# Performance work log

Measured on AMD Instinct MI355X. Metric: run time of the kernel, lower is better.

## Reference

```python
import jax, jax.numpy as jnp
import numpy as np

DIM = 2048
N_HEADS = 16
N_KV_HEADS = 4
HEAD_DIM = DIM // N_HEADS


def setup_inputs() -> dict:
    key = jax.random.key(0)
    k1, k2, k3, k4, k5 = jax.random.split(key, 5)
    B, T = 2, 2048
    scale = 1.0 / np.sqrt(DIM)
    x = jax.random.normal(k1, (B, T, DIM), dtype=jnp.float32)
    # weights stored as [in, out] so forward is x @ W (same math as nn.Linear)
    Wq = jax.random.normal(k2, (DIM, DIM), dtype=jnp.float32) * scale
    Wk = jax.random.normal(k3, (DIM, N_KV_HEADS * HEAD_DIM), dtype=jnp.float32) * scale
    Wv = jax.random.normal(k4, (DIM, N_KV_HEADS * HEAD_DIM), dtype=jnp.float32) * scale
    Wo = jax.random.normal(k5, (DIM, DIM), dtype=jnp.float32) * scale
    return {"x": x, "Wq": Wq, "Wk": Wk, "Wv": Wv, "Wo": Wo}


def reference(x, Wq, Wk, Wv, Wo):
    B, T, C = x.shape
    G = N_HEADS // N_KV_HEADS  # query heads per kv head
    # projections
    q = (x @ Wq).reshape(B, T, N_KV_HEADS, G, HEAD_DIM)   # [B,T,K,G,d]
    k = (x @ Wk).reshape(B, T, N_KV_HEADS, HEAD_DIM)      # [B,T,K,d]
    v = (x @ Wv).reshape(B, T, N_KV_HEADS, HEAD_DIM)      # [B,T,K,d]
    # attention scores: grouped heads share kv head (no repeat_interleave copy)
    att = jnp.einsum('btkgd,bskd->bkgts', q, k) / np.sqrt(HEAD_DIM)  # [B,K,G,T,T]
    att = jax.nn.softmax(att, axis=-1)
    out = jnp.einsum('bkgts,bskd->btkgd', att, v).reshape(B, T, C)
    return out @ Wo
```

## Files before the change

### kernel.cpp

```cpp
#include <hip/hip_runtime.h>
#include <hip/hip_bf16.h>

typedef __hip_bfloat16 bf16;
typedef __attribute__((ext_vector_type(8))) short short8;
typedef __attribute__((ext_vector_type(4))) short short4v;
typedef __attribute__((ext_vector_type(4))) float f32x4;

#define DIMC 2048
#define TSEQ 2048
#define NB 2
#define KVH 4
#define NH 16
#define HD 128
#define KVD 512
#define QSCALE 0.12751744f

#if __has_builtin(__builtin_amdgcn_exp2f)
#define EXP2(x) __builtin_amdgcn_exp2f(x)
#else
#define EXP2(x) exp2f(x)
#endif

__device__ __forceinline__ float fmax3(float a, float b, float c) {
  return fmaxf(fmaxf(a, b), c);
}

__device__ __forceinline__ void mfma16(f32x4& acc, short8 a, short8 b) {
  acc = __builtin_amdgcn_mfma_f32_16x16x32_bf16(a, b, acc, 0, 0, 0);
}

__device__ __forceinline__ void gload_lds16(const bf16* g, bf16* l) {
  __builtin_amdgcn_global_load_lds(
      (const __attribute__((address_space(1))) void*)g,
      (__attribute__((address_space(3))) void*)l, 16, 0, 0);
}

__device__ __forceinline__ int swz(int row, int col) {
  return col ^ ((row & 7) << 3);
}

__global__ __launch_bounds__(256) void f2b(const float* __restrict__ in,
                                           bf16* __restrict__ out, long n4) {
  long i = (long)blockIdx.x * 256 + threadIdx.x;
  if (i >= n4) return;
  const f32x4 v = *(const f32x4*)(in + i * 4);
  union { short4v s; bf16 h[4]; } u;
#pragma unroll
  for (int j = 0; j < 4; ++j) u.h[j] = __float2bfloat16(v[j]);
  *(short4v*)(out + i * 4) = u.s;
}

__global__ __launch_bounds__(256) void transpose_all(const float* __restrict__ Wq,
                                                     const float* __restrict__ Wk,
                                                     const float* __restrict__ Wv,
                                                     const float* __restrict__ Wo,
                                                     bf16* __restrict__ WT3,
                                                     bf16* __restrict__ WoT) {
  __shared__ bf16 tile[64][72];
  const int y = blockIdx.y;
  const float* in;
  bf16* out;
  int C, rb, cb;
  float scale = 1.0f;
  if (y < 32) {
    in = Wq; out = WT3; C = 2048;
    rb = y * 64; cb = blockIdx.x * 64; scale = QSCALE;
  } else if (y < 40) {
    in = Wk; out = WT3 + (long)2048 * DIMC; C = 512;
    rb = blockIdx.x * 64; cb = (y - 32) * 64;
  } else if (y < 48) {
    in = Wv; out = WT3 + (long)2560 * DIMC; C = 512;
    rb = blockIdx.x * 64; cb = (y - 40) * 64;
  } else {
    in = Wo; out = WoT; C = 2048;
    rb = (y - 48) * 64; cb = blockIdx.x * 64;
  }
  int tx = threadIdx.x & 63, ty = threadIdx.x >> 6;
  for (int i = ty; i < 64; i += 4)
    tile[i][tx] = __float2bfloat16(in[(long)(rb + i) * C + cb + tx] * scale);
  __syncthreads();
  for (int i = ty; i < 64; i += 4)
    out[(long)(cb + i) * DIMC + rb + tx] = tile[tx][i];
}

#define XCD_REMAP(NX)                                                          \
  const int flat_ = blockIdx.y * (NX) + blockIdx.x;                            \
  const int tot_ = (NX) * gridDim.y;                                           \
  const int log_ = (flat_ & 7) * (tot_ >> 3) + (flat_ >> 3);                   \
  const long m0 = (long)(log_ / (NX)) * 128, n0 = (long)(log_ % (NX)) * 128;

#define GEMM_BODY(A_, Bt_, K_)                                                  \
  const int tid = threadIdx.x;                                                  \
  const int lane = tid & 63, wid = tid >> 6;                                    \
  const int wm = (wid >> 1) * 64, wn = (wid & 1) * 64;                          \
  f32x4 acc[4][4] = {};                                                         \
  const int srow = lane >> 2, scol = (lane & 3) * 8;                            \
  const bf16* Ag = A_ + (m0 + srow) * (long)K_ + scol;                          \
  const bf16* Bg = Bt_ + (n0 + srow) * (long)K_ + scol;                         \
  for (int k0 = 0; k0 < K_; k0 += 32) {                                         \
    for (int p = 0; p < 2; ++p) {                                               \
      int rr = p * 64 + wid * 16;                                               \
      gload_lds16(Ag + (long)rr * K_ + k0, As + rr * 32);                       \
      gload_lds16(Bg + (long)rr * K_ + k0, Bs + rr * 32);                       \
    }                                                                           \
    __syncthreads();                                                            \
    const int ko = (lane >> 4) * 8;                                             \
    short8 af[4], bq[4];                                                        \
    _Pragma("unroll") for (int i = 0; i < 4; ++i) {                             \
      af[i] = *(const short8*)(As + (wm + i * 16 + (lane & 15)) * 32 + ko);     \
      bq[i] = *(const short8*)(Bs + (wn + i * 16 + (lane & 15)) * 32 + ko);     \
    }                                                                           \
    _Pragma("unroll") for (int i = 0; i < 4; ++i)                               \
      _Pragma("unroll") for (int j = 0; j < 4; ++j)                             \
        mfma16(acc[i][j], af[i], bq[j]);                                        \
    __syncthreads();                                                            \
  }                                                                             \
  const int cr = (lane >> 4) * 4, cc = lane & 15;

__global__ __launch_bounds__(256) void gemm_qkv(const bf16* __restrict__ A,
                                                const bf16* __restrict__ Bt,
                                                bf16* __restrict__ qp,
                                                bf16* __restrict__ kp,
                                                bf16* __restrict__ vT) {
  __shared__ bf16 As[128 * 32];
  __shared__ bf16 Bs[128 * 32];
  XCD_REMAP(24)
  GEMM_BODY(A, Bt, 2048)
#pragma unroll
  for (int i = 0; i < 4; ++i)
#pragma unroll
    for (int j = 0; j < 4; ++j)
#pragma unroll
      for (int r = 0; r < 4; ++r) {
        long m = m0 + wm + i * 16 + cr + r;
        long n = n0 + wn + j * 16 + cc;
        float val = acc[i][j][r];
        if (n0 < 2048) {
          qp[m * DIMC + n] = __float2bfloat16(val);
        } else if (n0 < 2560) {
          kp[m * KVD + (n - 2048)] = __float2bfloat16(val);
        } else {
          long nn = n - 2560;
          long z = (m >> 11) * 4 + (nn >> 7);
          vT[z * (HD * (long)TSEQ) + (nn & 127) * (long)TSEQ + (m & 2047)] =
              __float2bfloat16(val);
        }
      }
}

__global__ __launch_bounds__(256) void gemm_out(const bf16* __restrict__ A,
                                                const bf16* __restrict__ Bt,
                                                float* __restrict__ C) {
  __shared__ bf16 As[128 * 32];
  __shared__ bf16 Bs[128 * 32];
  XCD_REMAP(16)
  GEMM_BODY(A, Bt, 2048)
#pragma unroll
  for (int i = 0; i < 4; ++i)
#pragma unroll
    for (int j = 0; j < 4; ++j)
#pragma unroll
      for (int r = 0; r < 4; ++r) {
        long m = m0 + wm + i * 16 + cr + r;
        long n = n0 + wn + j * 16 + cc;
        C[m * DIMC + n] = acc[i][j][r];
      }
}

__global__ __launch_bounds__(256, 2) void attn_fwd(const bf16* __restrict__ Qp,
                                                   const bf16* __restrict__ Kp,
                                                   const bf16* __restrict__ Vt,
                                                   bf16* __restrict__ AO) {
  __shared__ bf16 Ks[2][64 * 128];
  __shared__ bf16 Vts[2][128 * 64];
  const int tid = threadIdx.x;
  const int lane = tid & 63, wid = tid >> 6;
  const int h = blockIdx.y, b = blockIdx.z;
  const int kv = h >> 2;
  const int t0 = blockIdx.x * 128;
  const int lr = lane & 15, lg = lane >> 4;

  short8 aq[2][4];
#pragma unroll
  for (int f = 0; f < 2; ++f) {
    const bf16* qrow =
        Qp + ((long)(b * TSEQ + t0 + wid * 32 + f * 16 + lr)) * DIMC + h * HD + lg * 8;
#pragma unroll
    for (int c = 0; c < 4; ++c) aq[f][c] = *(const short8*)(qrow + c * 32);
  }
  f32x4 o[2][8] = {};
  float mrun[2] = {-1e30f, -1e30f}, lrun[2] = {0.f, 0.f};

  const bf16* Kg = Kp + (long)b * TSEQ * KVD + kv * HD;
  const bf16* Vg = Vt + ((long)(b * KVH + kv)) * HD * TSEQ;

  const int krow = tid >> 2;
  const int vrow = tid >> 1;
  short8 kreg[2][2], vreg[2][2];
#pragma unroll
  for (int s = 0; s < 2; ++s)
#pragma unroll
    for (int p = 0; p < 2; ++p) {
      kreg[s][p] = *(const short8*)(Kg + (long)krow * KVD + (2 * (tid & 3) + s) * 16 + p * 8);
      vreg[s][p] = *(const short8*)(Vg + (long)vrow * TSEQ + (2 * (tid & 1) + s) * 16 + 8 * p);
    }

  for (int s0 = 0; s0 < TSEQ; s0 += 64) {
    const int buf = (s0 >> 6) & 1;
    bf16* Kb = Ks[buf];
    bf16* Vb = Vts[buf];
#pragma unroll
    for (int s = 0; s < 2; ++s)
#pragma unroll
      for (int p = 0; p < 2; ++p) {
        int kc0 = (2 * (tid & 3) + s) * 16;
        *(short8*)(Kb + krow * 128 + swz(krow, kc0 + p * 8)) = kreg[s][p];
        int va = 2 * (tid & 1) + s;
        union { short8 v8; short4v q[2]; } u;
        u.v8 = vreg[s][p];
        int sl1 = (4 * (va >> 1) + 2 * p + vrow) & 7;
        int sl2 = (4 * (va >> 1) + 2 * p + 1 + vrow) & 7;
        int hf = (va & 1) * 4;
        *(short4v*)(Vb + vrow * 64 + sl1 * 8 + hf) = u.q[0];
        *(short4v*)(Vb + vrow * 64 + sl2 * 8 + hf) = u.q[1];
      }
    __syncthreads();
    if (s0 + 64 < TSEQ) {
#pragma unroll
      for (int s = 0; s < 2; ++s)
#pragma unroll
        for (int p = 0; p < 2; ++p) {
          kreg[s][p] = *(const short8*)(Kg + (long)(s0 + 64 + krow) * KVD +
                                        (2 * (tid & 3) + s) * 16 + p * 8);
          vreg[s][p] = *(const short8*)(Vg + (long)vrow * TSEQ + s0 + 64 +
                                        (2 * (tid & 1) + s) * 16 + 8 * p);
        }
    }

    f32x4 sacc[2][4] = {};
    __builtin_amdgcn_s_setprio(1);
#pragma unroll
    for (int sf = 0; sf < 4; ++sf)
#pragma unroll
      for (int c = 0; c < 4; ++c) {
        int row = sf * 16 + lr;
        short8 kf = *(const short8*)(Kb + row * 128 + swz(row, c * 32 + lg * 8));
        mfma16(sacc[0][sf], kf, aq[0][c]);
        mfma16(sacc[1][sf], kf, aq[1][c]);
      }
    __builtin_amdgcn_s_setprio(0);

    union { short8 s; bf16 h[8]; } pb[2][2];
#pragma unroll
    for (int f = 0; f < 2; ++f) {
      float tmax = fmaxf(sacc[f][0][0], sacc[f][0][1]);
      tmax = fmax3(tmax, sacc[f][0][2], sacc[f][0][3]);
      tmax = fmax3(tmax, sacc[f][1][0], sacc[f][1][1]);
      tmax = fmax3(tmax, sacc[f][1][2], sacc[f][1][3]);
      tmax = fmax3(tmax, sacc[f][2][0], sacc[f][2][1]);
      tmax = fmax3(tmax, sacc[f][2][2], sacc[f][2][3]);
      tmax = fmax3(tmax, sacc[f][3][0], sacc[f][3][1]);
      tmax = fmax3(tmax, sacc[f][3][2], sacc[f][3][3]);
      tmax = fmaxf(tmax, __shfl_xor(tmax, 16));
      tmax = fmaxf(tmax, __shfl_xor(tmax, 32));
      if (__any(tmax > mrun[f] + 8.0f)) {
        float mnew = fmaxf(mrun[f], tmax);
        float fac = EXP2(mrun[f] - mnew);
        mrun[f] = mnew;
        lrun[f] *= fac;
#pragma unroll
        for (int df = 0; df < 8; ++df) o[f][df] *= fac;
      }
      float p4[4][4];
      float ps = 0.f;
#pragma unroll
      for (int sf = 0; sf < 4; ++sf)
#pragma unroll
        for (int r = 0; r < 4; ++r) {
          float pv = EXP2(sacc[f][sf][r] - mrun[f]);
          p4[sf][r] = pv;
          ps += pv;
        }
      lrun[f] += ps;
#pragma unroll
      for (int c2 = 0; c2 < 2; ++c2)
#pragma unroll
        for (int r = 0; r < 4; ++r) {
          pb[f][c2].h[r] = __float2bfloat16(p4[2 * c2][r]);
          pb[f][c2].h[4 + r] = __float2bfloat16(p4[2 * c2 + 1][r]);
        }
    }

    __builtin_amdgcn_s_setprio(1);
#pragma unroll
    for (int c2 = 0; c2 < 2; ++c2) {
#pragma unroll
      for (int df = 0; df < 8; ++df) {
        int row = df * 16 + lr;
        short8 vf = *(const short8*)(Vb + row * 64 + ((4 * c2 + lg + row) & 7) * 8);
        mfma16(o[0][df], vf, pb[0][c2].s);
        mfma16(o[1][df], vf, pb[1][c2].s);
      }
    }
    __builtin_amdgcn_s_setprio(0);
  }

#pragma unroll
  for (int f = 0; f < 2; ++f) {
    lrun[f] += __shfl_xor(lrun[f], 16);
    lrun[f] += __shfl_xor(lrun[f], 32);
  }

#pragma unroll
  for (int f = 0; f < 2; ++f) {
    float inv = 1.0f / lrun[f];
    bf16* obase =
        AO + ((long)(b * TSEQ + t0 + wid * 32 + f * 16 + lr)) * DIMC + h * HD + lg * 4;
#pragma unroll
    for (int df = 0; df < 8; ++df) {
      union { short4v s; bf16 h[4]; } ov;
#pragma unroll
      for (int r = 0; r < 4; ++r) ov.h[r] = __float2bfloat16(o[f][df][r] * inv);
      *(short4v*)(obase + df * 16) = ov.s;
    }
  }
}

extern "C" void kernel_launch(void* const* d_in, const int* in_sizes, int n_in,
                              void* d_out, int out_size, void* d_ws, size_t ws_size,
                              hipStream_t stream) {
  const float* x  = (const float*)d_in[0];
  const float* Wq = (const float*)d_in[1];
  const float* Wk = (const float*)d_in[2];
  const float* Wv = (const float*)d_in[3];
  const float* Wo = (const float*)d_in[4];
  float* out = (float*)d_out;
  bf16* ws = (bf16*)d_ws;

  bf16* xb  = ws;
  bf16* WT3 = xb + 8388608;
  bf16* WoT = WT3 + 6291456;
  bf16* qp  = WoT + 4194304;
  bf16* kp  = qp + 8388608;
  bf16* vT  = kp + 2097152;

  f2b<<<8192, 256, 0, stream>>>(x, xb, 2097152);
  transpose_all<<<dim3(32, 80), 256, 0, stream>>>(Wq, Wk, Wv, Wo, WT3, WoT);

  gemm_qkv<<<dim3(24, 32), 256, 0, stream>>>(xb, WT3, qp, kp, vT);

  bf16* ao = xb;
  attn_fwd<<<dim3(16, 16, 2), 256, 0, stream>>>(qp, kp, vT, ao);

  gemm_out<<<dim3(16, 32), 256, 0, stream>>>(ao, WoT, out);
}
```

Before: 221.0 us.

## Deepen GEMM K-tile to 64 with XOR-swizzled LDS and fuse x conversion into transpose

The shared GEMM body now stages a 64-wide K slice per iteration instead of 32. It uses an XOR swizzle on the LDS columns, applied both when loading and when reading, which halves the number of barriers per K and aims to avoid LDS bank conflicts on fragment reads. Separately, the x fp32-to-bf16 conversion is merged into the weight-transpose kernel as extra grid rows, which removes one kernel launch. LDS use per GEMM block doubles, which may reduce occupancy.

```diff
diff --git a/kernel.cpp b/kernel.cpp
--- a/kernel.cpp
+++ b/kernel.cpp
@@ -39,25 +39,29 @@
   return col ^ ((row & 7) << 3);
 }
 
-__global__ __launch_bounds__(256) void f2b(const float* __restrict__ in,
-                                           bf16* __restrict__ out, long n4) {
-  long i = (long)blockIdx.x * 256 + threadIdx.x;
-  if (i >= n4) return;
-  const f32x4 v = *(const f32x4*)(in + i * 4);
-  union { short4v s; bf16 h[4]; } u;
-#pragma unroll
-  for (int j = 0; j < 4; ++j) u.h[j] = __float2bfloat16(v[j]);
-  *(short4v*)(out + i * 4) = u.s;
-}
-
 __global__ __launch_bounds__(256) void transpose_all(const float* __restrict__ Wq,
                                                      const float* __restrict__ Wk,
                                                      const float* __restrict__ Wv,
                                                      const float* __restrict__ Wo,
+                                                     const float* __restrict__ x,
                                                      bf16* __restrict__ WT3,
-                                                     bf16* __restrict__ WoT) {
+                                                     bf16* __restrict__ WoT,
+                                                     bf16* __restrict__ xb) {
+  const int y = blockIdx.y;
+  if (y >= 80) {
+    long base = (((long)(y - 80) * 32 + blockIdx.x) * 2048) + threadIdx.x;
+#pragma unroll
+    for (int j = 0; j < 8; ++j) {
+      long i = base + j * 256;
+      const f32x4 v = *(const f32x4*)(x + i * 4);
+      union { short4v s; bf16 h[4]; } u;
+#pragma unroll
+      for (int k = 0; k < 4; ++k) u.h[k] = __float2bfloat16(v[k]);
+      *(short4v*)(xb + i * 4) = u.s;
+    }
+    return;
+  }
   __shared__ bf16 tile[64][72];
-  const int y = blockIdx.y;
   const float* in;
   bf16* out;
   int C, rb, cb;
@@ -94,25 +98,30 @@
   const int lane = tid & 63, wid = tid >> 6;                                    \
   const int wm = (wid >> 1) * 64, wn = (wid & 1) * 64;                          \
   f32x4 acc[4][4] = {};                                                         \
-  const int srow = lane >> 2, scol = (lane & 3) * 8;                            \
-  const bf16* Ag = A_ + (m0 + srow) * (long)K_ + scol;                          \
-  const bf16* Bg = Bt_ + (n0 + srow) * (long)K_ + scol;                         \
-  for (int k0 = 0; k0 < K_; k0 += 32) {                                         \
-    for (int p = 0; p < 2; ++p) {                                               \
-      int rr = p * 64 + wid * 16;                                               \
-      gload_lds16(Ag + (long)rr * K_ + k0, As + rr * 32);                       \
-      gload_lds16(Bg + (long)rr * K_ + k0, Bs + rr * 32);                       \
+  const int srow = lane >> 3;                  \
+  const int sslot = lane & 7;                           \
+  for (int k0 = 0; k0 < K_; k0 += 64) {                                         \
+    _Pragma("unroll") for (int p = 0; p < 4; ++p) {                             \
+      int rr = p * 32 + wid * 8;                                                \
+      int row = rr + srow;                                                      \
+      int scol = (sslot ^ (row & 7)) * 8;    \
+      gload_lds16(A_ + (m0 + row) * (long)K_ + k0 + scol, As + rr * 64);        \
+      gload_lds16(Bt_ + (n0 + row) * (long)K_ + k0 + scol, Bs + rr * 64);       \
     }                                                                           \
     __syncthreads();                                                            \
     const int ko = (lane >> 4) * 8;                                             \
-    short8 af[4], bq[4];                                                        \
-    _Pragma("unroll") for (int i = 0; i < 4; ++i) {                             \
-      af[i] = *(const short8*)(As + (wm + i * 16 + (lane & 15)) * 32 + ko);     \
-      bq[i] = *(const short8*)(Bs + (wn + i * 16 + (lane & 15)) * 32 + ko);     \
+    _Pragma("unroll") for (int kk = 0; kk < 2; ++kk) {                          \
+      short8 af[4], bq[4];                                                      \
+      _Pragma("unroll") for (int i = 0; i < 4; ++i) {                           \
+        int ra = wm + i * 16 + (lane & 15);                                     \
+        int rb2 = wn + i * 16 + (lane & 15);                                    \
+        af[i] = *(const short8*)(As + ra * 64 + swz(ra, kk * 32 + ko));         \
+        bq[i] = *(const short8*)(Bs + rb2 * 64 + swz(rb2, kk * 32 + ko));       \
+      }                                                                         \
+      _Pragma("unroll") for (int i = 0; i < 4; ++i)                             \
+        _Pragma("unroll") for (int j = 0; j < 4; ++j)                           \
+          mfma16(acc[i][j], af[i], bq[j]);                                      \
     }                                                                           \
-    _Pragma("unroll") for (int i = 0; i < 4; ++i)                               \
-      _Pragma("unroll") for (int j = 0; j < 4; ++j)                             \
-        mfma16(acc[i][j], af[i], bq[j]);                                        \
     __syncthreads();                                                            \
   }                                                                             \
   const int cr = (lane >> 4) * 4, cc = lane & 15;
@@ -122,8 +131,8 @@
                                                 bf16* __restrict__ qp,
                                                 bf16* __restrict__ kp,
                                                 bf16* __restrict__ vT) {
-  __shared__ bf16 As[128 * 32];
-  __shared__ bf16 Bs[128 * 32];
+  __shared__ bf16 As[128 * 64];
+  __shared__ bf16 Bs[128 * 64];
   XCD_REMAP(24)
   GEMM_BODY(A, Bt, 2048)
 #pragma unroll
@@ -151,8 +160,8 @@
 __global__ __launch_bounds__(256) void gemm_out(const bf16* __restrict__ A,
                                                 const bf16* __restrict__ Bt,
                                                 float* __restrict__ C) {
-  __shared__ bf16 As[128 * 32];
-  __shared__ bf16 Bs[128 * 32];
+  __shared__ bf16 As[128 * 64];
+  __shared__ bf16 Bs[128 * 64];
   XCD_REMAP(16)
   GEMM_BODY(A, Bt, 2048)
 #pragma unroll
@@ -344,8 +353,7 @@
   bf16* kp  = qp + 8388608;
   bf16* vT  = kp + 2097152;
 
-  f2b<<<8192, 256, 0, stream>>>(x, xb, 2097152);
-  transpose_all<<<dim3(32, 80), 256, 0, stream>>>(Wq, Wk, Wv, Wo, WT3, WoT);
+  transpose_all<<<dim3(32, 112), 256, 0, stream>>>(Wq, Wk, Wv, Wo, x, WT3, WoT, xb);
 
   gemm_qkv<<<dim3(24, 32), 256, 0, stream>>>(xb, WT3, qp, kp, vT);
 
```

Result: slower. 229.1 us (+3.7%).
